# Performance work log

Hardware: AMD Instinct MI355X
Metric: run time of the kernel (lower is better)

## Reference

```python
import jax, jax.numpy as jnp
import numpy as np

B, N, D, H = 2, 2048, 512, 8
HD = D // H
EPS = 1e-5


def layernorm(x, g, b):
    m = jnp.mean(x, axis=-1, keepdims=True)
    v = jnp.var(x, axis=-1, keepdims=True)
    return (x - m) * jax.lax.rsqrt(v + EPS) * g + b


def setup_inputs() -> dict:
    key = jax.random.key(0)
    ks = jax.random.split(key, 16)
    s = 1.0 / np.sqrt(D)
    def lin(k, din, dout):
        k1, k2 = jax.random.split(k)
        return (jax.random.uniform(k1, (din, dout), jnp.float32, -s, s),
                jax.random.uniform(k2, (dout,), jnp.float32, -s, s))
    Wq, bq = lin(ks[0], D, D)
    Wk, bk = lin(ks[1], D, D)
    Wv, bv = lin(ks[2], D, D)
    Wo, bo = lin(ks[3], D, D)
    W1, b1 = lin(ks[4], D, 2 * D)
    W2, b2 = lin(ks[5], 2 * D, D)
    return {
        'y': jax.random.normal(ks[6], (B, N, D), jnp.float32),
        'Wq': Wq, 'bq': bq, 'Wk': Wk, 'bk': bk, 'Wv': Wv, 'bv': bv,
        'Wo': Wo, 'bo': bo,
        'ln1_g': jnp.ones((D,)), 'ln1_b': jnp.zeros((D,)),
        'ln2_g': jnp.ones((D,)), 'ln2_b': jnp.zeros((D,)),
        'W1': W1, 'b1': b1, 'W2': W2, 'b2': b2,
    }


def reference(y, Wq, bq, Wk, bk, Wv, bv, Wo, bo, ln1_g, ln1_b, ln2_g, ln2_b, W1, b1, W2, b2):
    x = layernorm(y, ln1_g, ln1_b)
    def heads(W, b):
        return (x @ W + b).reshape(B, N, H, HD).transpose(0, 2, 1, 3)  # bhnc
    q = heads(Wq, bq)
    k = heads(Wk, bk)
    v = heads(Wv, bv)
    score = jax.nn.softmax(jnp.einsum('bhic,bhjc->bhij', q, k) / np.sqrt(HD), axis=-1)
    r = jnp.einsum('bhij,bhjc->bhic', score, v)
    r = r.transpose(0, 2, 1, 3).reshape(B, N, D) @ Wo + bo
    y = y + r
    h = layernorm(y, ln2_g, ln2_b)
    h = jax.nn.gelu(h @ W1 + b1, approximate=False) @ W2 + b2
    return y + h
```

## Files before the change

### kernel.cpp

```cpp
#include <hip/hip_runtime.h>

#define DEVI __device__ __forceinline__

typedef unsigned short u16;
typedef unsigned int   u32;
typedef unsigned long long u64;
typedef float  f32x4  __attribute__((ext_vector_type(4)));
typedef __bf16 bf16x8 __attribute__((ext_vector_type(8)));

union FragU { bf16x8 b; u64 u[2]; __bf16 e[8]; };

DEVI u16 f2b(float x) { __bf16 t = (__bf16)x; return __builtin_bit_cast(u16, t); }

DEVI float exp2a(float x) { float r; asm("v_exp_f32 %0, %1" : "=v"(r) : "v"(x)); return r; }

DEVI void gload16(const void* g, void* l) {
  __builtin_amdgcn_global_load_lds((const __attribute__((address_space(1))) u32*)g,
                                   (__attribute__((address_space(3))) u32*)l, 16, 0, 0);
}

DEVI int swzo(int row, int kb) {
  return ((((kb >> 4) ^ row) & 7) << 4) | ((kb ^ row) & 8) | (kb & 7);
}

DEVI u64 ldswz(const char* base, int row, int kb) {
  return *reinterpret_cast<const u64*>(base + row * 128 + swzo(row, kb));
}

DEVI size_t gaddr(int row, int kbyte, int rowbytes) {
  return (size_t)row * rowbytes + (size_t)((kbyte & ~127) + swzo(row, kbyte & 127));
}

__global__ __launch_bounds__(256)
void prep(const float* __restrict__ Wq, const float* __restrict__ Wk,
          const float* __restrict__ Wv, const float* __restrict__ Wo,
          const float* __restrict__ W1, const float* __restrict__ W2,
          u16* __restrict__ wqkvT, u16* __restrict__ woT,
          u16* __restrict__ w1T, u16* __restrict__ w2T,
          const float* __restrict__ y, const float* __restrict__ ln1g,
          const float* __restrict__ ln1b, char* __restrict__ xb) {
  const int id = blockIdx.x;
  if (id < 2048) {
    __shared__ float tile[32][33];
    const float* src; u16* dst; int K, N, bx, by;
    if (id < 1024) {
      const int m = id >> 8, t = id & 255;
      K = 512; N = 512; bx = t & 15; by = t >> 4;
      src = (m == 0) ? Wq : (m == 1) ? Wk : (m == 2) ? Wv : Wo;
      dst = (m == 3) ? woT : wqkvT + m * 512 * 512;
    } else if (id < 1536) {
      const int t = id - 1024; K = 512; N = 1024; bx = t & 31; by = t >> 5;
      src = W1; dst = w1T;
    } else {
      const int t = id - 1536; K = 1024; N = 512; bx = t & 15; by = t >> 4;
      src = W2; dst = w2T;
    }
    const int tx = threadIdx.x & 31, ty = threadIdx.x >> 5;
#pragma unroll
    for (int i = 0; i < 4; ++i)
      tile[ty + i * 8][tx] = src[(size_t)(by * 32 + ty + i * 8) * N + bx * 32 + tx];
    __syncthreads();
    const int nl = threadIdx.x >> 3, kq = threadIdx.x & 7;
    const int n = bx * 32 + nl;
    const int kg = by * 32 + kq * 4;
    union { ushort4 s; u64 q; } pk;
    pk.s.x = f2b(tile[kq * 4 + 0][nl]);
    pk.s.y = f2b(tile[kq * 4 + 1][nl]);
    pk.s.z = f2b(tile[kq * 4 + 2][nl]);
    pk.s.w = f2b(tile[kq * 4 + 3][nl]);
    *(u64*)((char*)dst + gaddr(n, 2 * kg, 2 * K)) = pk.q;
  } else {
    const int row = id - 2048;
    const int t = threadIdx.x;
    const float2 v = ((const float2*)(y + (size_t)row * 512))[t];
    float s1 = v.x + v.y, s2 = v.x * v.x + v.y * v.y;
#pragma unroll
    for (int off = 32; off; off >>= 1) { s1 += __shfl_xor(s1, off); s2 += __shfl_xor(s2, off); }
    __shared__ float a1[4], a2[4];
    const int w = t >> 6;
    if ((t & 63) == 0) { a1[w] = s1; a2[w] = s2; }
    __syncthreads();
    s1 = a1[0] + a1[1] + a1[2] + a1[3];
    s2 = a2[0] + a2[1] + a2[2] + a2[3];
    const float mean = s1 * (1.f / 512.f);
    const float var = s2 * (1.f / 512.f) - mean * mean;
    const float rstd = rsqrtf(var + 1e-5f);
    const float2 gg = ((const float2*)ln1g)[t];
    const float2 bb = ((const float2*)ln1b)[t];
    const u16 o0 = f2b((v.x - mean) * rstd * gg.x + bb.x);
    const u16 o1 = f2b((v.y - mean) * rstd * gg.y + bb.y);
    *(u32*)(xb + gaddr(row, 4 * t, 1024)) = (u32)o0 | ((u32)o1 << 16);
  }
}

__global__ __launch_bounds__(256)
void ln_bf16(const float* __restrict__ x, const float* __restrict__ g,
             const float* __restrict__ b, char* __restrict__ out) {
  const int row = blockIdx.x;
  const int t = threadIdx.x;
  const float2 v = ((const float2*)(x + (size_t)row * 512))[t];
  float s1 = v.x + v.y, s2 = v.x * v.x + v.y * v.y;
#pragma unroll
  for (int off = 32; off; off >>= 1) { s1 += __shfl_xor(s1, off); s2 += __shfl_xor(s2, off); }
  __shared__ float a1[4], a2[4];
  const int w = t >> 6;
  if ((t & 63) == 0) { a1[w] = s1; a2[w] = s2; }
  __syncthreads();
  s1 = a1[0] + a1[1] + a1[2] + a1[3];
  s2 = a2[0] + a2[1] + a2[2] + a2[3];
  const float mean = s1 * (1.f / 512.f);
  const float var = s2 * (1.f / 512.f) - mean * mean;
  const float rstd = rsqrtf(var + 1e-5f);
  const float2 gg = ((const float2*)g)[t];
  const float2 bb = ((const float2*)b)[t];
  const u16 o0 = f2b((v.x - mean) * rstd * gg.x + bb.x);
  const u16 o1 = f2b((v.y - mean) * rstd * gg.y + bb.y);
  *(u32*)(out + gaddr(row, 4 * t, 1024)) = (u32)o0 | ((u32)o1 << 16);
}

enum { EPI_QKV = 0, EPI_RES = 1, EPI_GELU = 2 };

template <int EPI, int WM, int WN, int AM, int AN>
__global__ __launch_bounds__(WM * WN * 64)
void gemm_bf16(const char* __restrict__ A, const char* __restrict__ Bt, int N, int K,
               const float* __restrict__ bias,
               const float* __restrict__ bq, const float* __restrict__ bk,
               const float* __restrict__ bv,
               const float* __restrict__ res, float* __restrict__ outF,
               char* __restrict__ outB,
               u16* __restrict__ qo, char* __restrict__ ko, char* __restrict__ vo) {
  constexpr int NW = WM * WN;
  constexpr int TM = WM * AM * 16, TN = WN * AN * 16;
  constexpr int NCHA = TM / 8, NCHB = TN / 8, NCH = NCHA + NCHB;
  constexpr int CPW = NCH / NW;
  static_assert(CPW * NW == NCH, "chunk split");
  __shared__ __align__(16) char sA[2][TM * 128];
  __shared__ __align__(16) char sB[2][TN * 128];
  const int tid = threadIdx.x;
  const int l = tid & 63, w = tid >> 6;
  const int tm = blockIdx.x, tn = blockIdx.y;
  const int wr = w / WN, wc = w % WN;
  const int u = l >> 4, r16 = l & 15;
  const int lrow = l >> 3, lgr = l & 7;
  f32x4 acc[AM][AN] = {};
  const size_t KB = (size_t)K * 2;
  const char* Ab = A + (size_t)(tm * TM) * KB;
  const char* Bb = Bt + (size_t)(tn * TN) * KB;
  const int nkt = K >> 6;
  auto stage = [&](int buf, int kt) {
#pragma unroll
    for (int i = 0; i < CPW; ++i) {
      const int c = w * CPW + i;
      if (c < NCHA) {
        gload16(Ab + (size_t)(c * 8 + lrow) * KB + (size_t)kt * 128 + (lgr << 4),
                sA[buf] + c * 1024);
      } else {
        const int c2 = c - NCHA;
        gload16(Bb + (size_t)(c2 * 8 + lrow) * KB + (size_t)kt * 128 + (lgr << 4),
                sB[buf] + c2 * 1024);
      }
    }
  };
  stage(0, 0);
  int cur = 0;
  for (int kt = 0; kt < nkt; ++kt) {
    __syncthreads();
    if (kt + 1 < nkt) stage(cur ^ 1, kt + 1);
    __builtin_amdgcn_s_setprio(1);
#pragma unroll
    for (int ks = 0; ks < 2; ++ks) {
      FragU af[AM], bfr[AN];
      const int kb = ks * 64 + (u << 3);
#pragma unroll
      for (int i = 0; i < AM; ++i) {
        af[i].u[0] = ldswz(sA[cur], wr * (AM * 16) + i * 16 + r16, kb);
        af[i].u[1] = ldswz(sA[cur], wr * (AM * 16) + i * 16 + r16, kb + 32);
      }
#pragma unroll
      for (int i = 0; i < AN; ++i) {
        bfr[i].u[0] = ldswz(sB[cur], wc * (AN * 16) + i * 16 + r16, kb);
        bfr[i].u[1] = ldswz(sB[cur], wc * (AN * 16) + i * 16 + r16, kb + 32);
      }
#pragma unroll
      for (int mi = 0; mi < AM; ++mi)
#pragma unroll
        for (int ni = 0; ni < AN; ++ni)
          acc[mi][ni] = __builtin_amdgcn_mfma_f32_16x16x32_bf16(af[mi].b, bfr[ni].b,
                                                                acc[mi][ni], 0, 0, 0);
    }
    __builtin_amdgcn_s_setprio(0);
    cur ^= 1;
  }
  const int row0 = tm * TM + wr * (AM * 16) + (u << 2);
  const int col0 = tn * TN + wc * (AN * 16) + r16;
#pragma unroll
  for (int mi = 0; mi < AM; ++mi) {
#pragma unroll
    for (int ni = 0; ni < AN; ++ni) {
      const int col = col0 + ni * 16;
      if (EPI == EPI_RES) {
#pragma unroll
        for (int r = 0; r < 4; ++r) {
          const int row = row0 + mi * 16 + r;
          outF[(size_t)row * N + col] = acc[mi][ni][r] + bias[col] + res[(size_t)row * N + col];
        }
      } else if (EPI == EPI_GELU) {
#pragma unroll
        for (int r = 0; r < 4; ++r) {
          const int row = row0 + mi * 16 + r;
          const float x = acc[mi][ni][r] + bias[col];
          *(u16*)(outB + gaddr(row, 2 * col, 2 * N)) =
              f2b(0.5f * x * (1.f + erff(x * 0.70710678118f)));
        }
      } else {
        const int which = col >> 9, cc = col & 511;
        const int h = cc >> 6, hd = cc & 63;
        if (which == 2) {
          const int rowa = row0 + mi * 16;
          const int bb2 = rowa >> 11, nt0 = rowa & 2047;
          const int bh = bb2 * 8 + h;
          const float bvv = bv[cc];
          union { ushort4 s; u64 q; } pk;
          pk.s.x = f2b(acc[mi][ni][0] + bvv);
          pk.s.y = f2b(acc[mi][ni][1] + bvv);
          pk.s.z = f2b(acc[mi][ni][2] + bvv);
          pk.s.w = f2b(acc[mi][ni][3] + bvv);
          *(u64*)(vo + (size_t)bh * 262144 + (size_t)(nt0 >> 6) * 8192 +
                  gaddr(hd, 2 * (nt0 & 63), 128)) = pk.q;
        } else {
#pragma unroll
          for (int r = 0; r < 4; ++r) {
            const int row = row0 + mi * 16 + r;
            const int bb2 = row >> 11, nt = row & 2047;
            const int bh = bb2 * 8 + h;
            if (which == 0)
              qo[((size_t)bh * 2048 + nt) * 64 + hd] = f2b((acc[mi][ni][r] + bq[cc]) * 0.18033688f);
            else
              *(u16*)(ko + (size_t)bh * 262144 + (size_t)(nt >> 6) * 8192 +
                      gaddr(nt & 63, 2 * hd, 128)) = f2b(acc[mi][ni][r] + bk[cc]);
          }
        }
      }
    }
  }
}

__global__ __launch_bounds__(512)
void attn_k(const u16* __restrict__ q, const char* __restrict__ kswz,
            const char* __restrict__ vswz, char* __restrict__ r_out) {
  __shared__ __align__(16) char sK[2][2][8192];
  __shared__ __align__(16) char sV[2][2][8192];
  const int tid = threadIdx.x;
  const int l = tid & 63, w = tid >> 6;
  const int kvh = w & 1, qw = w >> 1;
  const int bh = blockIdx.x, qt = blockIdx.y;
  const int u = l >> 4, r16 = l & 15;
  const char* kp = kswz + (size_t)bh * 262144;
  const char* vp = vswz + (size_t)bh * 262144;
  const int c0 = qw * 2;
  auto stage = [&](int buf, int t) {
#pragma unroll
    for (int c = 0; c < 2; ++c) {
      gload16(kp + (size_t)t * 8192 + (c0 + c) * 1024 + l * 16, sK[kvh][buf] + (c0 + c) * 1024);
      gload16(vp + (size_t)t * 8192 + (c0 + c) * 1024 + l * 16, sV[kvh][buf] + (c0 + c) * 1024);
    }
  };
  stage(0, kvh * 16);
  FragU qf[2], ones;
  {
    const u16* qr = q + (size_t)bh * (2048 * 64) + (size_t)(qt * 64 + qw * 16 + r16) * 64 + (u << 2);
    qf[0].u[0] = *(const u64*)qr;        qf[0].u[1] = *(const u64*)(qr + 16);
    qf[1].u[0] = *(const u64*)(qr + 32); qf[1].u[1] = *(const u64*)(qr + 48);
    ones.u[0] = 0x3F803F803F803F80ull;
    ones.u[1] = 0x3F803F803F803F80ull;
  }
  f32x4 o[4] = {};
  f32x4 lacc = {};
  int cur = 0;
  for (int i = 0; i < 16; ++i) {
    __syncthreads();
    if (i < 15) stage(cur ^ 1, kvh * 16 + i + 1);
    f32x4 st[4] = {};
    __builtin_amdgcn_s_setprio(1);
#pragma unroll
    for (int ks = 0; ks < 2; ++ks) {
      const int kb = ks * 64 + (u << 3);
#pragma unroll
      for (int mi = 0; mi < 4; ++mi) {
        FragU kf;
        kf.u[0] = ldswz(sK[kvh][cur], mi * 16 + r16, kb);
        kf.u[1] = ldswz(sK[kvh][cur], mi * 16 + r16, kb + 32);
        st[mi] = __builtin_amdgcn_mfma_f32_16x16x32_bf16(kf.b, qf[ks].b, st[mi], 0, 0, 0);
      }
    }
    __builtin_amdgcn_s_setprio(0);
#pragma unroll
    for (int mi = 0; mi < 4; ++mi)
#pragma unroll
      for (int r = 0; r < 4; ++r) st[mi][r] = exp2a(st[mi][r]);
    FragU pb[2];
#pragma unroll
    for (int ks = 0; ks < 2; ++ks)
#pragma unroll
      for (int j = 0; j < 4; ++j) {
        pb[ks].e[j]     = (__bf16)st[2 * ks][j];
        pb[ks].e[j + 4] = (__bf16)st[2 * ks + 1][j];
      }
    __builtin_amdgcn_s_setprio(1);
#pragma unroll
    for (int ks = 0; ks < 2; ++ks) {
      const int kb = ks * 64 + (u << 3);
      lacc = __builtin_amdgcn_mfma_f32_16x16x32_bf16(ones.b, pb[ks].b, lacc, 0, 0, 0);
#pragma unroll
      for (int mo = 0; mo < 4; ++mo) {
        FragU vf;
        vf.u[0] = ldswz(sV[kvh][cur], mo * 16 + r16, kb);
        vf.u[1] = ldswz(sV[kvh][cur], mo * 16 + r16, kb + 32);
        o[mo] = __builtin_amdgcn_mfma_f32_16x16x32_bf16(vf.b, pb[ks].b, o[mo], 0, 0, 0);
      }
    }
    __builtin_amdgcn_s_setprio(0);
    cur ^= 1;
  }
  __syncthreads();
  float* scrO = (float*)&sK[0][0][0];
  float* scrL = (float*)&sV[0][0][0];
  if (kvh == 1) {
    if (u == 0) scrL[qw * 32 + r16] = lacc[0];
#pragma unroll
    for (int mo = 0; mo < 4; ++mo)
#pragma unroll
      for (int r = 0; r < 4; ++r)
        scrO[qw * 1024 + (mo * 16 + u * 4 + r) * 16 + r16] = o[mo][r];
  }
  __syncthreads();
  if (kvh == 0) {
    const float linv = 1.f / (lacc[0] + scrL[qw * 32 + r16]);
    const int tok = (bh >> 3) * 2048 + qt * 64 + qw * 16 + r16;
    const int h = bh & 7;
#pragma unroll
    for (int mo = 0; mo < 4; ++mo) {
      union { ushort4 s; u64 qq; } pk;
      float vv[4];
#pragma unroll
      for (int r = 0; r < 4; ++r)
        vv[r] = (o[mo][r] + scrO[qw * 1024 + (mo * 16 + u * 4 + r) * 16 + r16]) * linv;
      pk.s.x = f2b(vv[0]); pk.s.y = f2b(vv[1]); pk.s.z = f2b(vv[2]); pk.s.w = f2b(vv[3]);
      *(u64*)(r_out + (size_t)tok * 1024 + h * 128 + swzo(tok, mo * 32 + (u << 3))) = pk.qq;
    }
  }
}

extern "C" void kernel_launch(void* const* d_in, const int* in_sizes, int n_in,
                              void* d_out, int out_size, void* d_ws, size_t ws_size,
                              hipStream_t stream) {
  const float* y    = (const float*)d_in[0];
  const float* Wq   = (const float*)d_in[1];
  const float* bq   = (const float*)d_in[2];
  const float* Wk   = (const float*)d_in[3];
  const float* bk   = (const float*)d_in[4];
  const float* Wv   = (const float*)d_in[5];
  const float* bv   = (const float*)d_in[6];
  const float* Wo   = (const float*)d_in[7];
  const float* bo   = (const float*)d_in[8];
  const float* ln1g = (const float*)d_in[9];
  const float* ln1b = (const float*)d_in[10];
  const float* ln2g = (const float*)d_in[11];
  const float* ln2b = (const float*)d_in[12];
  const float* W1   = (const float*)d_in[13];
  const float* b1   = (const float*)d_in[14];
  const float* W2   = (const float*)d_in[15];
  const float* b2   = (const float*)d_in[16];
  float* out = (float*)d_out;
  char* ws = (char*)d_ws;
  char* xb    = ws;
  u16*  qb    = (u16*)(ws + (4u << 20));
  char* kswz  = ws + (8u << 20);
  char* vswz  = ws + (12u << 20);
  char* rb    = ws + (16u << 20);
  char* g1b   = ws + (20u << 20);
  u16* wqkvT  = (u16*)(ws + (28u << 20));
  u16* woT    = wqkvT + 1536 * 512;
  u16* w1T    = woT + 512 * 512;
  u16* w2T    = w1T + 1024 * 512;

  prep<<<6144, 256, 0, stream>>>(Wq, Wk, Wv, Wo, W1, W2, wqkvT, woT, w1T, w2T,
                                 y, ln1g, ln1b, xb);
  gemm_bf16<EPI_QKV, 2, 2, 4, 2><<<dim3(32, 24), 256, 0, stream>>>(
      xb, (const char*)wqkvT, 1536, 512, nullptr, bq, bk, bv,
      nullptr, nullptr, nullptr, qb, kswz, vswz);
  attn_k<<<dim3(16, 32), 512, 0, stream>>>(qb, kswz, vswz, rb);
  gemm_bf16<EPI_RES, 2, 2, 2, 2><<<dim3(64, 8), 256, 0, stream>>>(
      rb, (const char*)woT, 512, 512, bo, nullptr, nullptr, nullptr,
      y, out, nullptr, nullptr, nullptr, nullptr);
  ln_bf16<<<4096, 256, 0, stream>>>(out, ln2g, ln2b, xb);
  gemm_bf16<EPI_GELU, 2, 2, 4, 2><<<dim3(32, 16), 256, 0, stream>>>(
      xb, (const char*)w1T, 1024, 512, b1, nullptr, nullptr, nullptr,
      nullptr, nullptr, g1b, nullptr, nullptr, nullptr);
  gemm_bf16<EPI_RES, 2, 2, 2, 2><<<dim3(64, 8), 256, 0, stream>>>(
      g1b, (const char*)w2T, 512, 1024, b2, nullptr, nullptr, nullptr,
      out, out, nullptr, nullptr, nullptr, nullptr);
}
```

Measured before the change: 94.58 us.

## Split attention key tiles into 32-key steps with separate K/V staging

The attention loop now walks 32 key steps of 32 keys each instead of 16 steps of 64. K is double-buffered per 32-key step, and V is still staged per 64 keys and reused across two steps. This halves K shared memory and the score registers per step, which may lower register and LDS pressure and shorten the exp-to-PV dependency chain. The cost is twice as many block-wide barriers and less MFMA work between them, so latency hiding could get worse.

```diff
diff --git a/kernel.cpp b/kernel.cpp
--- a/kernel.cpp
+++ b/kernel.cpp
@@ -248,7 +248,7 @@
 __global__ __launch_bounds__(512)
 void attn_k(const u16* __restrict__ q, const char* __restrict__ kswz,
             const char* __restrict__ vswz, char* __restrict__ r_out) {
-  __shared__ __align__(16) char sK[2][2][8192];
+  __shared__ __align__(16) char sK[2][2][4096];
   __shared__ __align__(16) char sV[2][2][8192];
   const int tid = threadIdx.x;
   const int l = tid & 63, w = tid >> 6;
@@ -257,15 +257,18 @@
   const int u = l >> 4, r16 = l & 15;
   const char* kp = kswz + (size_t)bh * 262144;
   const char* vp = vswz + (size_t)bh * 262144;
-  const int c0 = qw * 2;
-  auto stage = [&](int buf, int t) {
-#pragma unroll
-    for (int c = 0; c < 2; ++c) {
-      gload16(kp + (size_t)t * 8192 + (c0 + c) * 1024 + l * 16, sK[kvh][buf] + (c0 + c) * 1024);
-      gload16(vp + (size_t)t * 8192 + (c0 + c) * 1024 + l * 16, sV[kvh][buf] + (c0 + c) * 1024);
-    }
+  auto stageK = [&](int buf, int s) {
+    const int t = kvh * 32 + s;
+    const size_t g = (size_t)(t >> 1) * 8192 + (size_t)(t & 1) * 4096;
+    gload16(kp + g + qw * 1024 + l * 16, sK[kvh][buf] + qw * 1024);
   };
-  stage(0, kvh * 16);
+  auto stageV = [&](int buf, int j) {
+    const size_t g = (size_t)(kvh * 16 + j) * 8192 + qw * 2048;
+    gload16(vp + g + l * 16,        sV[kvh][buf] + qw * 2048);
+    gload16(vp + g + 1024 + l * 16, sV[kvh][buf] + qw * 2048 + 1024);
+  };
+  stageK(0, 0);
+  stageV(0, 0);
   FragU qf[2], ones;
   {
     const u16* qr = q + (size_t)bh * (2048 * 64) + (size_t)(qt * 64 + qw * 16 + r16) * 64 + (u << 2);
@@ -276,51 +279,46 @@
   }
   f32x4 o[4] = {};
   f32x4 lacc = {};
-  int cur = 0;
-  for (int i = 0; i < 16; ++i) {
+  for (int i = 0; i < 32; ++i) {
+    const int kcur = i & 1, vcur = (i >> 1) & 1;
     __syncthreads();
-    if (i < 15) stage(cur ^ 1, kvh * 16 + i + 1);
-    f32x4 st[4] = {};
+    if (i + 1 < 32) stageK(kcur ^ 1, i + 1);
+    if ((i & 1) == 0 && (i >> 1) + 1 < 16) stageV(vcur ^ 1, (i >> 1) + 1);
+    f32x4 st[2] = {};
     __builtin_amdgcn_s_setprio(1);
 #pragma unroll
     for (int ks = 0; ks < 2; ++ks) {
       const int kb = ks * 64 + (u << 3);
 #pragma unroll
-      for (int mi = 0; mi < 4; ++mi) {
+      for (int mi = 0; mi < 2; ++mi) {
         FragU kf;
-        kf.u[0] = ldswz(sK[kvh][cur], mi * 16 + r16, kb);
-        kf.u[1] = ldswz(sK[kvh][cur], mi * 16 + r16, kb + 32);
+        kf.u[0] = ldswz(sK[kvh][kcur], mi * 16 + r16, kb);
+        kf.u[1] = ldswz(sK[kvh][kcur], mi * 16 + r16, kb + 32);
         st[mi] = __builtin_amdgcn_mfma_f32_16x16x32_bf16(kf.b, qf[ks].b, st[mi], 0, 0, 0);
       }
     }
     __builtin_amdgcn_s_setprio(0);
 #pragma unroll
-    for (int mi = 0; mi < 4; ++mi)
+    for (int mi = 0; mi < 2; ++mi)
 #pragma unroll
       for (int r = 0; r < 4; ++r) st[mi][r] = exp2a(st[mi][r]);
-    FragU pb[2];
-#pragma unroll
-    for (int ks = 0; ks < 2; ++ks)
-#pragma unroll
-      for (int j = 0; j < 4; ++j) {
-        pb[ks].e[j]     = (__bf16)st[2 * ks][j];
-        pb[ks].e[j + 4] = (__bf16)st[2 * ks + 1][j];
-      }
+    FragU pb;
+#pragma unroll
+    for (int j = 0; j < 4; ++j) {
+      pb.e[j]     = (__bf16)st[0][j];
+      pb.e[j + 4] = (__bf16)st[1][j];
+    }
+    const int kb0 = (i & 1) * 64 + (u << 3);
     __builtin_amdgcn_s_setprio(1);
-#pragma unroll
-    for (int ks = 0; ks < 2; ++ks) {
-      const int kb = ks * 64 + (u << 3);
-      lacc = __builtin_amdgcn_mfma_f32_16x16x32_bf16(ones.b, pb[ks].b, lacc, 0, 0, 0);
-#pragma unroll
-      for (int mo = 0; mo < 4; ++mo) {
-        FragU vf;
-        vf.u[0] = ldswz(sV[kvh][cur], mo * 16 + r16, kb);
-        vf.u[1] = ldswz(sV[kvh][cur], mo * 16 + r16, kb + 32);
-        o[mo] = __builtin_amdgcn_mfma_f32_16x16x32_bf16(vf.b, pb[ks].b, o[mo], 0, 0, 0);
-      }
+    lacc = __builtin_amdgcn_mfma_f32_16x16x32_bf16(ones.b, pb.b, lacc, 0, 0, 0);
+#pragma unroll
+    for (int mo = 0; mo < 4; ++mo) {
+      FragU vf;
+      vf.u[0] = ldswz(sV[kvh][vcur], mo * 16 + r16, kb0);
+      vf.u[1] = ldswz(sV[kvh][vcur], mo * 16 + r16, kb0 + 32);
+      o[mo] = __builtin_amdgcn_mfma_f32_16x16x32_bf16(vf.b, pb.b, o[mo], 0, 0, 0);
     }
     __builtin_amdgcn_s_setprio(0);
-    cur ^= 1;
   }
   __syncthreads();
   float* scrO = (float*)&sK[0][0][0];
```

After: 99.66 us. 1.05x slower.
